# Optimization experiments

Hardware: AMD Instinct MI355X
Metric: run time of the kernel (lower is better)

Reference implementation:

```python
import jax, jax.numpy as jnp
import numpy as np

N_HEADS = 6
HEAD_SIZE = 64


def setup_inputs() -> dict:
    key = jax.random.key(0)
    k1, k2, k3, k4 = jax.random.split(key, 4)
    B, T, C = 8, 2048, N_HEADS * HEAD_SIZE
    x = jax.random.normal(k1, (B, T, C), dtype=jnp.float32)
    # small init scale keeps softmax logits in a sane range
    w_qkv = jax.random.normal(k2, (C, 3 * C), dtype=jnp.float32) * 0.05
    w_proj = jax.random.normal(k3, (C, C), dtype=jnp.float32) * 0.05
    b_proj = jax.random.normal(k4, (C,), dtype=jnp.float32) * 0.05
    return {"x": x, "w_qkv": w_qkv, "w_proj": w_proj, "b_proj": b_proj}


def reference(x, w_qkv, w_proj, b_proj):
    B, T, C = x.shape
    qkv = x @ w_qkv                      # [B, T, 3C]
    q, k, v = jnp.split(qkv, 3, axis=2)
    # [B, T, C] -> [B, H, T, D]
    def heads(t):
        return t.reshape(B, T, N_HEADS, HEAD_SIZE).transpose(0, 2, 1, 3)
    q, k, v = heads(q), heads(k), heads(v)
    scale = HEAD_SIZE ** -0.5
    scores = jnp.einsum('bhqd,bhkd->bhqk', q, k) * scale   # [B, H, T, T]
    causal = jnp.tril(jnp.ones((T, T), dtype=bool))
    scores = jnp.where(causal[None, None], scores, jnp.float32(-jnp.inf))
    weights = jax.nn.softmax(scores, axis=-1)
    # dropout is identity in eval mode
    out = jnp.einsum('bhqk,bhkd->bhqd', weights, v)          # [B, H, T, D]
    out = out.transpose(0, 2, 1, 3).reshape(B, T, C)
    return out @ w_proj + b_proj
```

## Files before the change

### kernel.cpp

```cpp
#include <hip/hip_runtime.h>
#include <hip/hip_bf16.h>

typedef __bf16 bf16_t;
typedef __bf16 bf16x8 __attribute__((ext_vector_type(8)));
typedef __bf16 bf16x4 __attribute__((ext_vector_type(4)));
typedef float floatx4 __attribute__((ext_vector_type(4)));
typedef unsigned uint32x2 __attribute__((ext_vector_type(2)));

#define MFMA16(a, b, c) __builtin_amdgcn_mfma_f32_16x16x32_bf16(a, b, c, 0, 0, 0)

#if __has_builtin(__builtin_amdgcn_exp2f)
#define EXP2F(x) __builtin_amdgcn_exp2f(x)
#else
#define EXP2F(x) __expf((x)*0.693147180559945f)
#endif

__device__ __forceinline__ void async_copy16(const bf16_t* g, bf16_t* l) {
    __builtin_amdgcn_global_load_lds((const __attribute__((address_space(1))) void*)g,
                                     (__attribute__((address_space(3))) void*)l, 16, 0, 0);
}

__device__ __forceinline__ unsigned cvt_pk_bf16(float lo, float hi) {
    unsigned r;
    asm("v_cvt_pk_bf16_f32 %0, %1, %2" : "=v"(r) : "v"(lo), "v"(hi));
    return r;
}

__device__ __forceinline__ void plane32(unsigned& x, unsigned& y) {
#if __has_builtin(__builtin_amdgcn_permlane32_swap)
    uint32x2 r = __builtin_amdgcn_permlane32_swap(x, y, false, false);
    x = r[0]; y = r[1];
#else
    asm("v_permlane32_swap_b32 %0, %1" : "+v"(x), "+v"(y));
#endif
}
__device__ __forceinline__ void plane16(unsigned& x, unsigned& y) {
#if __has_builtin(__builtin_amdgcn_permlane16_swap)
    uint32x2 r = __builtin_amdgcn_permlane16_swap(x, y, false, false);
    x = r[0]; y = r[1];
#else
    asm("v_permlane16_swap_b32 %0, %1" : "+v"(x), "+v"(y));
#endif
}

__device__ __forceinline__ bf16x8 pack_pfrag(const floatx4& sE, const floatx4& sO) {
    unsigned a0 = cvt_pk_bf16(sE[0], sE[1]);
    unsigned a1 = cvt_pk_bf16(sE[2], sE[3]);
    unsigned b0 = cvt_pk_bf16(sO[0], sO[1]);
    unsigned b1 = cvt_pk_bf16(sO[2], sO[3]);
    plane32(a0, b0);
    plane32(a1, b1);
    plane16(a0, b0);
    plane16(a1, b1);
    union { unsigned u[4]; bf16x8 v; } r;
    r.u[0] = a0; r.u[1] = a1; r.u[2] = b0; r.u[3] = b1;
    return r.v;
}

__global__ void prep_fused(const float* __restrict__ x, const float* __restrict__ w_qkv,
                           const float* __restrict__ w_proj, bf16_t* __restrict__ xb,
                           bf16_t* __restrict__ wqkvT, bf16_t* __restrict__ wprojT) {
    const int bx = blockIdx.x, tid = threadIdx.x;
    if (bx < 3072) {
        size_t i = ((size_t)bx * 256 + tid) * 8;
        float4 v0 = *(const float4*)(x + i);
        float4 v1 = *(const float4*)(x + i + 4);
        bf16x8 o = {(bf16_t)v0.x, (bf16_t)v0.y, (bf16_t)v0.z, (bf16_t)v0.w,
                    (bf16_t)v1.x, (bf16_t)v1.y, (bf16_t)v1.z, (bf16_t)v1.w};
        *(bf16x8*)(xb + i) = o;
        return;
    }
    __shared__ float tile[32][33];
    int which, n0, k0, Nd;
    if (bx < 3072 + 432) {
        int idx = bx - 3072;
        which = 0; Nd = 1152; n0 = (idx % 36) * 32; k0 = (idx / 36) * 32;
    } else {
        int idx = bx - 3072 - 432;
        which = 1; Nd = 384; n0 = (idx % 12) * 32; k0 = (idx / 12) * 32;
    }
    const float* in = which ? w_proj : w_qkv;
    bf16_t* out = which ? wprojT : wqkvT;
    const int tx = tid & 31, ty = tid >> 5;
#pragma unroll
    for (int i = 0; i < 4; i++)
        tile[ty + i * 8][tx] = in[(size_t)(k0 + ty + i * 8) * Nd + n0 + tx];
    __syncthreads();
#pragma unroll
    for (int i = 0; i < 4; i++) {
        int n = n0 + ty + i * 8;
        float v = tile[tx][ty + i * 8];
        if (!which && n < 384) v *= 0.1803368851f;
        out[(size_t)n * 384 + k0 + tx] = (bf16_t)v;
    }
}

__global__ __launch_bounds__(256, 3)
void gemm_qkv(const bf16_t* __restrict__ A, const bf16_t* __restrict__ Bt,
              bf16_t* __restrict__ qkv, bf16_t* __restrict__ Vt, int M, int N, int K) {
    __shared__ __align__(16) bf16_t As[2][128 * 32];
    __shared__ __align__(16) bf16_t Bs[2][128 * 32];
    const int nblk = blockIdx.x;
    const int wgl = ((nblk & 7) * 144) + (nblk >> 3);
    const int row0 = (wgl / 9) * 128, col0 = (wgl % 9) * 128;
    const int tid = threadIdx.x;
    const int wave = tid >> 6, lane = tid & 63;
    const int wm = wave >> 1, wn = wave & 1;
    const int quad = lane >> 4, l16 = lane & 15;
    const int swz = l16 & 3;

    floatx4 acc[4][4];
#pragma unroll
    for (int i = 0; i < 4; i++)
#pragma unroll
        for (int j = 0; j < 4; j++) acc[i][j] = (floatx4){0.f, 0.f, 0.f, 0.f};

    auto stage = [&](int buf, int k0) {
#pragma unroll
        for (int it = 0; it < 2; it++) {
            int cb = wave * 64 + it * 256;
            int c = cb + lane;
            int r = c >> 2;
            int col = k0 + (((c & 3) ^ (r & 3)) * 8);
            async_copy16(A + (size_t)(row0 + r) * K + col, &As[buf][0] + cb * 8);
            async_copy16(Bt + (size_t)(col0 + r) * K + col, &Bs[buf][0] + cb * 8);
        }
    };

    const int nk = K >> 5;
    stage(0, 0);
    for (int kt = 0; kt < nk; kt++) {
        __syncthreads();
        if (kt + 1 < nk) stage((kt + 1) & 1, (kt + 1) * 32);
        const bf16_t* as = &As[kt & 1][0];
        const bf16_t* bs = &Bs[kt & 1][0];
        bf16x8 af[4], bfr[4];
#pragma unroll
        for (int i = 0; i < 4; i++)
            af[i] = *(const bf16x8*)(as + (wm * 64 + i * 16 + l16) * 32 + ((quad ^ swz) * 8));
#pragma unroll
        for (int j = 0; j < 4; j++)
            bfr[j] = *(const bf16x8*)(bs + (wn * 64 + j * 16 + l16) * 32 + ((quad ^ swz) * 8));
#pragma unroll
        for (int i = 0; i < 4; i++)
#pragma unroll
            for (int j = 0; j < 4; j++) acc[i][j] = MFMA16(bfr[j], af[i], acc[i][j]);
    }
    if (col0 < 768) {
#pragma unroll
        for (int i = 0; i < 4; i++) {
            const size_t row = (size_t)(row0 + wm * 64 + i * 16 + l16);
#pragma unroll
            for (int j = 0; j < 4; j++) {
                const int colb = col0 + wn * 64 + j * 16 + quad * 4;
                bf16x4 v = {(bf16_t)acc[i][j][0], (bf16_t)acc[i][j][1],
                            (bf16_t)acc[i][j][2], (bf16_t)acc[i][j][3]};
                *(bf16x4*)(qkv + row * N + colb) = v;
            }
        }
    } else {
        __syncthreads();
        bf16_t* myb = &As[0][0] + wave * 4096;
#pragma unroll
        for (int i = 0; i < 4; i++)
#pragma unroll
            for (int j = 0; j < 4; j++)
#pragma unroll
                for (int r = 0; r < 4; r++) {
                    int d2 = j * 16 + quad * 4 + r;
                    int t2 = i * 16 + l16;
                    myb[d2 * 64 + (((t2 >> 3) ^ (d2 & 7)) * 8) + (t2 & 7)] =
                        (bf16_t)acc[i][j][r];
                }
        asm volatile("s_waitcnt lgkmcnt(0)" ::: "memory");
        const int row_t = row0 + wm * 64;
        const int b = row_t >> 11;
        const int tt = (row_t & 2047) >> 6;
        const int h = (col0 - 768 + wn * 64) >> 6;
        bf16_t* vout = Vt + (((size_t)(b * 6 + h) * 32 + tt) << 12);
#pragma unroll
        for (int it = 0; it < 8; it++) {
            int d2 = it * 8 + (lane >> 3);
            int cl = lane & 7;
            bf16x8 v = *(const bf16x8*)(myb + d2 * 64 + ((cl ^ (d2 & 7)) * 8));
            *(bf16x8*)(vout + d2 * 64 + cl * 8) = v;
        }
    }
}

__global__ __launch_bounds__(256, 3)
void gemm_out(const bf16_t* __restrict__ A, const bf16_t* __restrict__ Bt,
              float* __restrict__ C, int M, int N, int K, const float* __restrict__ bias) {
    __shared__ __align__(16) bf16_t As[2][64 * 32];
    __shared__ __align__(16) bf16_t Bs[2][128 * 32];
    const int nblk = blockIdx.x;
    const int wgl = ((nblk & 7) * 96) + (nblk >> 3);
    const int row0 = (wgl / 3) * 64, col0 = (wgl % 3) * 128;
    const int tid = threadIdx.x;
    const int wave = tid >> 6, lane = tid & 63;
    const int wm = wave >> 1, wn = wave & 1;
    const int quad = lane >> 4, l16 = lane & 15;
    const int swz = l16 & 3;

    floatx4 acc[2][4];
#pragma unroll
    for (int i = 0; i < 2; i++)
#pragma unroll
        for (int j = 0; j < 4; j++) acc[i][j] = (floatx4){0.f, 0.f, 0.f, 0.f};

    auto stage = [&](int buf, int k0) {
        {
            int c = wave * 64 + lane;
            int r = c >> 2;
            int col = k0 + (((c & 3) ^ (r & 3)) * 8);
            async_copy16(A + (size_t)(row0 + r) * K + col, &As[buf][0] + (wave * 64) * 8);
        }
#pragma unroll
        for (int it = 0; it < 2; it++) {
            int cb = wave * 64 + it * 256;
            int c = cb + lane;
            int r = c >> 2;
            int col = k0 + (((c & 3) ^ (r & 3)) * 8);
            async_copy16(Bt + (size_t)(col0 + r) * K + col, &Bs[buf][0] + cb * 8);
        }
    };

    const int nk = K >> 5;
    stage(0, 0);
    for (int kt = 0; kt < nk; kt++) {
        __syncthreads();
        if (kt + 1 < nk) stage((kt + 1) & 1, (kt + 1) * 32);
        const bf16_t* as = &As[kt & 1][0];
        const bf16_t* bs = &Bs[kt & 1][0];
        bf16x8 af[2], bfr[4];
#pragma unroll
        for (int i = 0; i < 2; i++)
            af[i] = *(const bf16x8*)(as + (wm * 32 + i * 16 + l16) * 32 + ((quad ^ swz) * 8));
#pragma unroll
        for (int j = 0; j < 4; j++)
            bfr[j] = *(const bf16x8*)(bs + (wn * 64 + j * 16 + l16) * 32 + ((quad ^ swz) * 8));
#pragma unroll
        for (int i = 0; i < 2; i++)
#pragma unroll
            for (int j = 0; j < 4; j++) acc[i][j] = MFMA16(bfr[j], af[i], acc[i][j]);
    }
#pragma unroll
    for (int i = 0; i < 2; i++) {
        const size_t row = (size_t)(row0 + wm * 32 + i * 16 + l16);
#pragma unroll
        for (int j = 0; j < 4; j++) {
            const int colb = col0 + wn * 64 + j * 16 + quad * 4;
            float4 bv = *(const float4*)(bias + colb);
            float4 v = {acc[i][j][0] + bv.x, acc[i][j][1] + bv.y,
                        acc[i][j][2] + bv.z, acc[i][j][3] + bv.w};
            *(float4*)(C + row * N + colb) = v;
        }
    }
}

__device__ __forceinline__ void stage64(const bf16_t* __restrict__ gtile, int stride,
                                        bf16_t* lds, int wave, int lane) {
#pragma unroll
    for (int it = 0; it < 2; it++) {
        int cb = wave * 64 + it * 256;
        int c = cb + lane;
        int r = c >> 3;
        int col = ((c & 7) ^ (r & 7)) * 8;
        async_copy16(gtile + (size_t)r * stride + col, lds + cb * 8);
    }
}

__global__ __launch_bounds__(256, 3)
void attn_kernel(const bf16_t* __restrict__ qkv, const bf16_t* __restrict__ Vt,
                 bf16_t* __restrict__ attn_out) {
    constexpr int T = 2048, C3 = 1152;
    const int nblk = blockIdx.x;
    const int wgl = ((nblk & 7) * 96) + (nblk >> 3);
    const int bx = wgl & 15;
    const int g = wgl >> 4;
    const int h = g % 6, b = g / 6;
    const int qa = bx, qb = 31 - bx;
    const int tid = threadIdx.x;
    const int wave = tid >> 6, lane = tid & 63;
    const int quad = lane >> 4, l16 = lane & 15;

    __shared__ __align__(16) bf16_t Ks[2][64 * 64];
    __shared__ __align__(16) bf16_t Vs[2][64 * 64];

    const bf16_t* kbase = qkv + (size_t)b * T * C3 + 384 + h * 64;
    const bf16_t* vbase = Vt + (((size_t)(b * 6 + h) * 32) << 12);

    const bf16_t* qpa =
        qkv + ((size_t)b * T + qa * 64 + wave * 16 + l16) * C3 + h * 64 + quad * 8;
    const bf16_t* qpb =
        qkv + ((size_t)b * T + qb * 64 + wave * 16 + l16) * C3 + h * 64 + quad * 8;
    bf16x8 qA0 = *(const bf16x8*)qpa, qA1 = *(const bf16x8*)(qpa + 32);
    bf16x8 qB0 = *(const bf16x8*)qpb, qB1 = *(const bf16x8*)(qpb + 32);

    floatx4 oA[4], oB[4];
    float lpA = 0.f, lpB = 0.f;
#pragma unroll
    for (int r = 0; r < 4; r++) {
        oA[r] = (floatx4){0.f, 0.f, 0.f, 0.f};
        oB[r] = (floatx4){0.f, 0.f, 0.f, 0.f};
    }
    const floatx4 C0 = {-13.f, -13.f, -13.f, -13.f};

    stage64(kbase, C3, &Ks[0][0], wave, lane);
    stage64(vbase, 64, &Vs[0][0], wave, lane);

    const int swz = l16 & 7;

    for (int kt = 0; kt <= qb; kt++) {
        __syncthreads();
        if (kt < qb) {
            stage64(kbase + (size_t)(kt + 1) * 64 * C3, C3, &Ks[(kt + 1) & 1][0], wave, lane);
            stage64(vbase + ((kt + 1) << 12), 64, &Vs[(kt + 1) & 1][0], wave, lane);
        }
        const bf16_t* kb = &Ks[kt & 1][0];
        const bf16_t* vb = &Vs[kt & 1][0];
        const bool doA = (kt <= qa);

        bf16x8 kf[4][2];
#pragma unroll
        for (int nt = 0; nt < 4; nt++)
#pragma unroll
            for (int hh = 0; hh < 2; hh++)
                kf[nt][hh] = *(const bf16x8*)(kb + (nt * 16 + l16) * 64 +
                                              (((hh * 4 + quad) ^ swz) * 8));

        floatx4 sA[4], sB[4];
        __builtin_amdgcn_s_setprio(1);
#pragma unroll
        for (int nt = 0; nt < 4; nt++) {
            sB[nt] = MFMA16(kf[nt][0], qB0, C0);
            sB[nt] = MFMA16(kf[nt][1], qB1, sB[nt]);
        }
        if (doA) {
#pragma unroll
            for (int nt = 0; nt < 4; nt++) {
                sA[nt] = MFMA16(kf[nt][0], qA0, C0);
                sA[nt] = MFMA16(kf[nt][1], qA1, sA[nt]);
            }
        }
        __builtin_amdgcn_s_setprio(0);

        bf16x8 vf[4][2];
#pragma unroll
        for (int nt = 0; nt < 4; nt++)
#pragma unroll
            for (int hh = 0; hh < 2; hh++)
                vf[nt][hh] = *(const bf16x8*)(vb + (nt * 16 + l16) * 64 +
                                              (((hh * 4 + quad) ^ swz) * 8));

        if (kt == qb) {
#pragma unroll
            for (int nt = 0; nt < 4; nt++)
#pragma unroll
                for (int r = 0; r < 4; r++)
                    if (nt * 16 + quad * 4 + r > wave * 16 + l16) sB[nt][r] = -1e30f;
        }
        if (kt == qa) {
#pragma unroll
            for (int nt = 0; nt < 4; nt++)
#pragma unroll
                for (int r = 0; r < 4; r++)
                    if (nt * 16 + quad * 4 + r > wave * 16 + l16) sA[nt][r] = -1e30f;
        }

#pragma unroll
        for (int nt = 0; nt < 4; nt++)
#pragma unroll
            for (int r = 0; r < 4; r++) {
                float p = EXP2F(sB[nt][r]);
                sB[nt][r] = p;
                lpB += p;
            }
        bf16x8 pB0 = pack_pfrag(sB[0], sB[1]);
        bf16x8 pB1 = pack_pfrag(sB[2], sB[3]);

        bf16x8 pA0, pA1;
        if (doA) {
#pragma unroll
            for (int nt = 0; nt < 4; nt++)
#pragma unroll
                for (int r = 0; r < 4; r++) {
                    float p = EXP2F(sA[nt][r]);
                    sA[nt][r] = p;
                    lpA += p;
                }
            pA0 = pack_pfrag(sA[0], sA[1]);
            pA1 = pack_pfrag(sA[2], sA[3]);
        }

        __builtin_amdgcn_s_setprio(1);
#pragma unroll
        for (int dt = 0; dt < 4; dt++) {
            oB[dt] = MFMA16(vf[dt][0], pB0, oB[dt]);
            oB[dt] = MFMA16(vf[dt][1], pB1, oB[dt]);
        }
        if (doA) {
#pragma unroll
            for (int dt = 0; dt < 4; dt++) {
                oA[dt] = MFMA16(vf[dt][0], pA0, oA[dt]);
                oA[dt] = MFMA16(vf[dt][1], pA1, oA[dt]);
            }
        }
        __builtin_amdgcn_s_setprio(0);
    }

    lpA += __shfl_xor(lpA, 16); lpA += __shfl_xor(lpA, 32);
    lpB += __shfl_xor(lpB, 16); lpB += __shfl_xor(lpB, 32);
    const float invA = 1.0f / lpA, invB = 1.0f / lpB;
    const int tA = qa * 64 + wave * 16 + l16, tB = qb * 64 + wave * 16 + l16;
#pragma unroll
    for (int dt = 0; dt < 4; dt++) {
        bf16x4 va = {(bf16_t)(oA[dt][0] * invA), (bf16_t)(oA[dt][1] * invA),
                     (bf16_t)(oA[dt][2] * invA), (bf16_t)(oA[dt][3] * invA)};
        bf16x4 vb4 = {(bf16_t)(oB[dt][0] * invB), (bf16_t)(oB[dt][1] * invB),
                      (bf16_t)(oB[dt][2] * invB), (bf16_t)(oB[dt][3] * invB)};
        int col = h * 64 + dt * 16 + quad * 4;
        *(bf16x4*)(attn_out + ((size_t)b * T + tA) * 384 + col) = va;
        *(bf16x4*)(attn_out + ((size_t)b * T + tB) * 384 + col) = vb4;
    }
}

extern "C" void kernel_launch(void* const* d_in, const int* in_sizes, int n_in,
                              void* d_out, int out_size, void* d_ws, size_t ws_size,
                              hipStream_t stream) {
    const float* x      = (const float*)d_in[0];
    const float* w_qkv  = (const float*)d_in[1];
    const float* w_proj = (const float*)d_in[2];
    const float* b_proj = (const float*)d_in[3];
    float* out = (float*)d_out;

    bf16_t* ws = (bf16_t*)d_ws;
    bf16_t* wqkvT = ws;
    bf16_t* wprojT = wqkvT + 1152 * 384;
    bf16_t* xb = wprojT + 384 * 384;
    bf16_t* qkv = xb + (size_t)16384 * 384;
    bf16_t* Vt = qkv + (size_t)16384 * 1152;
    bf16_t* attn = Vt + (size_t)48 * 64 * 2048;

    hipLaunchKernelGGL(prep_fused, dim3(3072 + 432 + 144), dim3(256), 0, stream,
                       x, w_qkv, w_proj, xb, wqkvT, wprojT);
    hipLaunchKernelGGL(gemm_qkv, dim3(1152), dim3(256), 0, stream,
                       xb, wqkvT, qkv, Vt, 16384, 1152, 384);
    hipLaunchKernelGGL(attn_kernel, dim3(768), dim3(256), 0, stream, qkv, Vt, attn);
    hipLaunchKernelGGL(gemm_out, dim3(768), dim3(256), 0, stream,
                       attn, wprojT, out, 16384, 384, 384, b_proj);
}
```

Baseline: 169.4 us.

## Split attention workgroups into two KV-range halves with a separate normalization kernel

Each former workgroup, which handled a paired low/high query tile over the full key range, is now split into two workgroups. One handles the diagonal part: the low tile plus the high tile's keys up to qa. The other handles the remaining key tiles for the high query tile. Because a fixed max offset is used instead of a running max, the partial unnormalized outputs and row sums are written in fp32 to scratch and combined by a new attn_norm kernel. This doubles the grid and raises the occupancy hint for better load balance on the GPU, at the cost of an extra launch and fp32 partial traffic.

Measured after the change: 380.9 us. 2.25x slower.

```diff
diff --git a/kernel.cpp b/kernel.cpp
--- a/kernel.cpp
+++ b/kernel.cpp
@@ -270,16 +270,22 @@
     }
 }
 
-__global__ __launch_bounds__(256, 3)
+__global__ __launch_bounds__(256, 5)
 void attn_kernel(const bf16_t* __restrict__ qkv, const bf16_t* __restrict__ Vt,
-                 bf16_t* __restrict__ attn_out) {
+                 bf16_t* __restrict__ attn_out, float* __restrict__ Opart,
+                 float* __restrict__ Lpart) {
     constexpr int T = 2048, C3 = 1152;
-    const int nblk = blockIdx.x;
-    const int wgl = ((nblk & 7) * 96) + (nblk >> 3);
-    const int bx = wgl & 15;
-    const int g = wgl >> 4;
+    const int n = blockIdx.x;
+    const int xcd = n & 7, i = n >> 3;
+    const int j = i / 6, gl = i % 6;
+    const int g = xcd * 6 + gl;
     const int h = g % 6, b = g / 6;
-    const int qa = bx, qb = 31 - bx;
+    const bool isD = (0x6AD5AB50u >> j) & 1;
+    const int c = (int)((j < 16 ? (0x98A7B6CD5E4F3210ull >> (4 * j))
+                                : (0xF01E2D3C45B6A798ull >> (4 * (j - 16)))) & 15);
+    const int qa = c, qb = 31 - c;
+    const int kt0 = isD ? 0 : (c + 1);
+    const int kt1 = isD ? qa : qb;
     const int tid = threadIdx.x;
     const int wave = tid >> 6, lane = tid & 63;
     const int quad = lane >> 4, l16 = lane & 15;
@@ -290,12 +296,15 @@
     const bf16_t* kbase = qkv + (size_t)b * T * C3 + 384 + h * 64;
     const bf16_t* vbase = Vt + (((size_t)(b * 6 + h) * 32) << 12);
 
-    const bf16_t* qpa =
-        qkv + ((size_t)b * T + qa * 64 + wave * 16 + l16) * C3 + h * 64 + quad * 8;
     const bf16_t* qpb =
         qkv + ((size_t)b * T + qb * 64 + wave * 16 + l16) * C3 + h * 64 + quad * 8;
-    bf16x8 qA0 = *(const bf16x8*)qpa, qA1 = *(const bf16x8*)(qpa + 32);
     bf16x8 qB0 = *(const bf16x8*)qpb, qB1 = *(const bf16x8*)(qpb + 32);
+    bf16x8 qA0, qA1;
+    if (isD) {
+        const bf16_t* qpa =
+            qkv + ((size_t)b * T + qa * 64 + wave * 16 + l16) * C3 + h * 64 + quad * 8;
+        qA0 = *(const bf16x8*)qpa; qA1 = *(const bf16x8*)(qpa + 32);
+    }
 
     floatx4 oA[4], oB[4];
     float lpA = 0.f, lpB = 0.f;
@@ -306,20 +315,20 @@
     }
     const floatx4 C0 = {-13.f, -13.f, -13.f, -13.f};
 
-    stage64(kbase, C3, &Ks[0][0], wave, lane);
-    stage64(vbase, 64, &Vs[0][0], wave, lane);
+    stage64(kbase + (size_t)kt0 * 64 * C3, C3, &Ks[kt0 & 1][0], wave, lane);
+    stage64(vbase + ((size_t)kt0 << 12), 64, &Vs[kt0 & 1][0], wave, lane);
 
     const int swz = l16 & 7;
 
-    for (int kt = 0; kt <= qb; kt++) {
+    for (int kt = kt0; kt <= kt1; kt++) {
         __syncthreads();
-        if (kt < qb) {
+        if (kt < kt1) {
             stage64(kbase + (size_t)(kt + 1) * 64 * C3, C3, &Ks[(kt + 1) & 1][0], wave, lane);
-            stage64(vbase + ((kt + 1) << 12), 64, &Vs[(kt + 1) & 1][0], wave, lane);
+            stage64(vbase + ((size_t)(kt + 1) << 12), 64, &Vs[(kt + 1) & 1][0], wave, lane);
         }
         const bf16_t* kb = &Ks[kt & 1][0];
         const bf16_t* vb = &Vs[kt & 1][0];
-        const bool doA = (kt <= qa);
+        const bool doA = isD;
 
         bf16x8 kf[4][2];
 #pragma unroll
@@ -360,7 +369,7 @@
                 for (int r = 0; r < 4; r++)
                     if (nt * 16 + quad * 4 + r > wave * 16 + l16) sB[nt][r] = -1e30f;
         }
-        if (kt == qa) {
+        if (doA && kt == qa) {
 #pragma unroll
             for (int nt = 0; nt < 4; nt++)
 #pragma unroll
@@ -409,20 +418,61 @@
         __builtin_amdgcn_s_setprio(0);
     }
 
-    lpA += __shfl_xor(lpA, 16); lpA += __shfl_xor(lpA, 32);
     lpB += __shfl_xor(lpB, 16); lpB += __shfl_xor(lpB, 32);
-    const float invA = 1.0f / lpA, invB = 1.0f / lpB;
-    const int tA = qa * 64 + wave * 16 + l16, tB = qb * 64 + wave * 16 + l16;
+
+    if (isD) {
+        lpA += __shfl_xor(lpA, 16); lpA += __shfl_xor(lpA, 32);
+        const float invA = 1.0f / lpA;
+        const int tA = qa * 64 + wave * 16 + l16;
+#pragma unroll
+        for (int dt = 0; dt < 4; dt++) {
+            bf16x4 va = {(bf16_t)(oA[dt][0] * invA), (bf16_t)(oA[dt][1] * invA),
+                         (bf16_t)(oA[dt][2] * invA), (bf16_t)(oA[dt][3] * invA)};
+            int col = h * 64 + dt * 16 + quad * 4;
+            *(bf16x4*)(attn_out + ((size_t)b * T + tA) * 384 + col) = va;
+        }
+    }
+
+    const int slot = isD ? 0 : 1;
+    const size_t tile_id = ((size_t)g * 16 + (qb - 16)) * 2 + slot;
+    const size_t pb = (tile_id * 64 + (wave * 16 + l16)) * 64;
 #pragma unroll
     for (int dt = 0; dt < 4; dt++) {
-        bf16x4 va = {(bf16_t)(oA[dt][0] * invA), (bf16_t)(oA[dt][1] * invA),
-                     (bf16_t)(oA[dt][2] * invA), (bf16_t)(oA[dt][3] * invA)};
-        bf16x4 vb4 = {(bf16_t)(oB[dt][0] * invB), (bf16_t)(oB[dt][1] * invB),
-                      (bf16_t)(oB[dt][2] * invB), (bf16_t)(oB[dt][3] * invB)};
-        int col = h * 64 + dt * 16 + quad * 4;
-        *(bf16x4*)(attn_out + ((size_t)b * T + tA) * 384 + col) = va;
-        *(bf16x4*)(attn_out + ((size_t)b * T + tB) * 384 + col) = vb4;
-    }
+        float4 v = {oB[dt][0], oB[dt][1], oB[dt][2], oB[dt][3]};
+        *(float4*)(Opart + pb + dt * 16 + quad * 4) = v;
+    }
+    if (quad == 0) Lpart[tile_id * 64 + wave * 16 + l16] = lpB;
+}
+
+__global__ __launch_bounds__(256)
+void attn_norm(const float* __restrict__ Opart, const float* __restrict__ Lpart,
+               bf16_t* __restrict__ attn_out) {
+    constexpr int T = 2048;
+    const int n = blockIdx.x;
+    const int xcd = n & 7, i = n >> 3;
+    const int gl = i % 6, tq = i / 6;
+    const int g = xcd * 6 + gl;
+    const int h = g % 6, b = g / 6;
+    const int tid = threadIdx.x;
+    const int r = tid >> 2, d0 = (tid & 3) * 16;
+    const size_t t2 = ((size_t)g * 16 + tq) * 2;
+    const float lp = Lpart[t2 * 64 + r] + Lpart[(t2 + 1) * 64 + r];
+    const float inv = 1.0f / lp;
+    const size_t b0 = ((t2 + 0) * 64 + r) * 64 + d0;
+    const size_t b1 = ((t2 + 1) * 64 + r) * 64 + d0;
+    bf16_t ov[16];
+#pragma unroll
+    for (int cchunk = 0; cchunk < 4; cchunk++) {
+        float4 x0 = *(const float4*)(Opart + b0 + cchunk * 4);
+        float4 x1 = *(const float4*)(Opart + b1 + cchunk * 4);
+        ov[cchunk * 4 + 0] = (bf16_t)((x0.x + x1.x) * inv);
+        ov[cchunk * 4 + 1] = (bf16_t)((x0.y + x1.y) * inv);
+        ov[cchunk * 4 + 2] = (bf16_t)((x0.z + x1.z) * inv);
+        ov[cchunk * 4 + 3] = (bf16_t)((x0.w + x1.w) * inv);
+    }
+    bf16_t* dst = attn_out + ((size_t)b * T + 1024 + tq * 64 + r) * 384 + h * 64 + d0;
+    *(bf16x8*)(dst) = *(bf16x8*)(ov);
+    *(bf16x8*)(dst + 8) = *(bf16x8*)(ov + 8);
 }
 
 extern "C" void kernel_launch(void* const* d_in, const int* in_sizes, int n_in,
@@ -441,12 +491,16 @@
     bf16_t* qkv = xb + (size_t)16384 * 384;
     bf16_t* Vt = qkv + (size_t)16384 * 1152;
     bf16_t* attn = Vt + (size_t)48 * 64 * 2048;
+    float* Opart = (float*)(attn + (size_t)16384 * 384);
+    float* Lpart = Opart + (size_t)48 * 16 * 2 * 64 * 64;
 
     hipLaunchKernelGGL(prep_fused, dim3(3072 + 432 + 144), dim3(256), 0, stream,
                        x, w_qkv, w_proj, xb, wqkvT, wprojT);
     hipLaunchKernelGGL(gemm_qkv, dim3(1152), dim3(256), 0, stream,
                        xb, wqkvT, qkv, Vt, 16384, 1152, 384);
-    hipLaunchKernelGGL(attn_kernel, dim3(768), dim3(256), 0, stream, qkv, Vt, attn);
+    hipLaunchKernelGGL(attn_kernel, dim3(1536), dim3(256), 0, stream,
+                       qkv, Vt, attn, Opart, Lpart);
+    hipLaunchKernelGGL(attn_norm, dim3(768), dim3(256), 0, stream, Opart, Lpart, attn);
     hipLaunchKernelGGL(gemm_out, dim3(768), dim3(256), 0, stream,
                        attn, wprojT, out, 16384, 384, 384, b_proj);
 }
```
